# Optimization experiments

Hardware: AMD Instinct MI355X
Metric: run time of the kernel (lower is better)

## Reference

```python
import jax, jax.numpy as jnp
import numpy as np

B, N, DIM, HEADS, DHEAD, DEPTH, EDGE = 1, 384, 128, 4, 64, 3, 8
INNER = HEADS * DHEAD  # 256


def _make_rotary():
    inv = 1.0 / (10000.0 ** (np.arange(0, DHEAD, 2, dtype=np.float32) / DHEAD))
    f = np.arange(N, dtype=np.float32)[:, None] * inv[None, :]  # [N, DHEAD//2]
    f = np.repeat(f, 2, axis=-1)  # interleaved pairs -> [N, DHEAD]
    return jnp.asarray(np.cos(f)), jnp.asarray(np.sin(f))

COS, SIN = _make_rotary()


def _rotate_half(x):
    x2 = x.reshape(x.shape[:-1] + (DHEAD // 2, 2))
    return jnp.stack((-x2[..., 1], x2[..., 0]), axis=-1).reshape(x.shape)


def _layer_norm(x, s, b, eps=1e-3):
    mu = jnp.mean(x, axis=-1, keepdims=True)
    var = jnp.mean(jnp.square(x - mu), axis=-1, keepdims=True)
    return (x - mu) * jax.lax.rsqrt(var + eps) * s + b


def _gated_res(x, res, Wg):
    gi = jnp.concatenate([x, res, x - res], axis=-1)  # [B,N,3*DIM]
    g = jax.nn.sigmoid(gi @ Wg)  # [B,N,1]
    return x * g + res * (1.0 - g)


def setup_inputs() -> dict:
    key = jax.random.key(0)
    ks = jax.random.split(key, 16)
    p = lambda k, shape: 0.02 * jax.random.normal(k, shape, jnp.float32)
    return {
        "nodes": jax.random.normal(ks[0], (B, N, DIM), jnp.float32),
        "edges": jax.random.normal(ks[1], (B, N, N, EDGE), jnp.float32),
        "ln1_s": jnp.ones((DEPTH, DIM), jnp.float32), "ln1_b": jnp.zeros((DEPTH, DIM), jnp.float32),
        "Wq": p(ks[2], (DEPTH, DIM, INNER)), "bq": jnp.zeros((DEPTH, INNER), jnp.float32),
        "Wkv": p(ks[3], (DEPTH, DIM, 2 * INNER)), "bkv": jnp.zeros((DEPTH, 2 * INNER), jnp.float32),
        "We": p(ks[4], (DEPTH, EDGE, INNER)), "be": jnp.zeros((DEPTH, INNER), jnp.float32),
        "Wo": p(ks[5], (DEPTH, INNER, DIM)), "bo": jnp.zeros((DEPTH, DIM), jnp.float32),
        "Wg_attn": p(ks[6], (DEPTH, 3 * DIM, 1)),
        "ln2_s": jnp.ones((DEPTH, DIM), jnp.float32), "ln2_b": jnp.zeros((DEPTH, DIM), jnp.float32),
        "W1": p(ks[7], (DEPTH, DIM, 4 * DIM)), "b1": jnp.zeros((DEPTH, 4 * DIM), jnp.float32),
        "W2": p(ks[8], (DEPTH, 4 * DIM, DIM)), "b2": jnp.zeros((DEPTH, DIM), jnp.float32),
        "Wg_ff": p(ks[9], (DEPTH, 3 * DIM, 1)),
        "Wd1": p(ks[10], (DIM, 9)), "bd1": jnp.zeros((9,), jnp.float32),
        "Wd2": p(ks[11], (9, 3)), "bd2": jnp.zeros((3,), jnp.float32),
        "mask": jnp.ones((B, N), dtype=bool),
    }


def _forward(nodes, edges, ln1_s, ln1_b, Wq, bq, Wkv, bkv, We, be, Wo, bo, Wg_attn,
             ln2_s, ln2_b, W1, b1, W2, b2, Wg_ff, Wd1, bd1, Wd2, bd2, mask):
    cos = COS[None, None]  # [1,1,N,DHEAD]
    sin = SIN[None, None]
    mask2 = mask[:, None, :, None] & mask[:, None, None, :]  # [B,1,N,N]
    x = nodes
    for i in range(DEPTH):
        # --- pre-norm attention with edge-conditioned K/V and rotary pos emb ---
        xn = _layer_norm(x, ln1_s[i], ln1_b[i])
        q = (xn @ Wq[i] + bq[i]).reshape(B, N, HEADS, DHEAD).transpose(0, 2, 1, 3)
        k, v = jnp.split(xn @ Wkv[i] + bkv[i], 2, axis=-1)
        k = k.reshape(B, N, HEADS, DHEAD).transpose(0, 2, 1, 3)
        v = v.reshape(B, N, HEADS, DHEAD).transpose(0, 2, 1, 3)
        e = (edges @ We[i] + be[i]).reshape(B, N, N, HEADS, DHEAD).transpose(0, 3, 1, 2, 4)  # [B,H,i,j,d]
        q = q * cos + _rotate_half(q) * sin
        k = k * cos + _rotate_half(k) * sin
        kf = k[:, :, None, :, :] + e  # [B,H,i,j,d]
        vf = v[:, :, None, :, :] + e
        sim = jnp.einsum('bhid,bhijd->bhij', q, kf) * (DHEAD ** -0.5)
        sim = jnp.where(mask2, sim, -1e9)
        attn = jax.nn.softmax(sim, axis=-1)
        out = jnp.einsum('bhij,bhijd->bhid', attn, vf)
        out = out.transpose(0, 2, 1, 3).reshape(B, N, INNER) @ Wo[i] + bo[i]
        x = _gated_res(out, x, Wg_attn[i])
        # --- pre-norm feedforward ---
        xn2 = _layer_norm(x, ln2_s[i], ln2_b[i])
        h = jax.nn.gelu(xn2 @ W1[i] + b1[i], approximate=False)
        ff = h @ W2[i] + b2[i]
        x = _gated_res(ff, x, Wg_ff[i])
    y = jax.nn.relu(x @ Wd1 + bd1)
    y = y @ Wd2 + bd2  # [B,N,3]
    return y - jnp.mean(y, axis=1)  # broadcasts since B == 1 (matches TF semantics)


def reference(nodes, edges, ln1_s, ln1_b, Wq, bq, Wkv, bkv, We, be, Wo, bo, Wg_attn,
              ln2_s, ln2_b, W1, b1, W2, b2, Wg_ff, Wd1, bd1, Wd2, bd2, mask):
    return _forward(nodes, edges, ln1_s, ln1_b, Wq, bq, Wkv, bkv, We, be, Wo, bo, Wg_attn,
                    ln2_s, ln2_b, W1, b1, W2, b2, Wg_ff, Wd1, bd1, Wd2, bd2, mask)
```

## Files before the change

### kernel.cpp

```cpp
#include <hip/hip_runtime.h>
#include <math.h>

#define NTOK 384
#define DIM  128
#define HEADS 4
#define DHEAD 64
#define INNER 256
#define DEPTH 3
#define EDGE 8
#define FFD 512

__device__ __forceinline__ float wave_sum64(float v){
#pragma unroll
  for (int m = 32; m >= 1; m >>= 1) v += __shfl_xor(v, m, 64);
  return v;
}
__device__ __forceinline__ float wave_max64(float v){
#pragma unroll
  for (int m = 32; m >= 1; m >>= 1) v = fmaxf(v, __shfl_xor(v, m, 64));
  return v;
}

__device__ __forceinline__ int swz_row(int id){ return (id & 7) * 48 + (id >> 3); }

__device__ __forceinline__ void rotary_val(int i, int d, float* c, float* s){
  int j = d >> 1;
  double ex = (double)(2 * j) / 64.0;
  float p = (float)pow(10000.0, ex);
  float inv = 1.0f / p;
  float f = (float)i * inv;
  double fd = (double)f;
  *c = (float)cos(fd);
  *s = (float)sin(fd);
}

__device__ __forceinline__ void qkv_row_v2(
    int i, int t, const float* __restrict__ snx,
    const float* __restrict__ Wq, const float* __restrict__ bq,
    const float* __restrict__ Wkv, const float* __restrict__ bkv,
    const float* __restrict__ We, const float* __restrict__ be,
    const float* __restrict__ cosRow, const float* __restrict__ sinRow,
    float* __restrict__ qb_, float* __restrict__ kbT, float* __restrict__ vb_,
    float* __restrict__ qWeB, float* __restrict__ qbeB,
    float4* __restrict__ qp4)
{
  int ks   = (t < 192) ? 0 : 1;
  int quad = (t < 192) ? t : t - 192;
  float4 acc = {0.f, 0.f, 0.f, 0.f};
  if (t < 384){
    const float4* Wp; int stride4;
    if (quad < 64){ Wp = (const float4*)Wq + quad;         stride4 = 64;  }
    else          { Wp = (const float4*)Wkv + (quad - 64); stride4 = 128; }
    int k0 = ks * 64;
#pragma unroll 8
    for (int kk = 0; kk < 64; ++kk){
      int k = k0 + kk;
      float4 w = Wp[(size_t)k * stride4];
      float x = snx[k];
      acc.x = fmaf(x, w.x, acc.x); acc.y = fmaf(x, w.y, acc.y);
      acc.z = fmaf(x, w.z, acc.z); acc.w = fmaf(x, w.w, acc.w);
    }
    if (ks == 1) qp4[quad] = acc;
  }
  __syncthreads();
  if (t < 192){
    float4 p = qp4[quad];
    acc.x += p.x; acc.y += p.y; acc.z += p.z; acc.w += p.w;
    if (quad < 64){
      int c0 = 4 * quad;
      float4 b = ((const float4*)bq)[quad];
      float a0 = acc.x + b.x, a1 = acc.y + b.y, a2 = acc.z + b.z, a3 = acc.w + b.w;
      int d0 = c0 & 63;
      float c_0 = cosRow[d0],     s_0 = sinRow[d0];
      float c_1 = cosRow[d0 + 2], s_1 = sinRow[d0 + 2];
      float r0 = a0 * c_0 - a1 * s_0;
      float r1 = a1 * c_0 + a0 * s_0;
      float r2 = a2 * c_1 - a3 * s_1;
      float r3 = a3 * c_1 + a2 * s_1;
      float4 qv; qv.x = r0; qv.y = r1; qv.z = r2; qv.w = r3;
      *(float4*)(qb_ + (size_t)i * 256 + c0) = qv;
      int h = quad >> 4;
#pragma unroll
      for (int cc = 0; cc < 8; ++cc){
        const float* wc = We + cc * 256 + c0;
        float pr = r0 * wc[0] + r1 * wc[1] + r2 * wc[2] + r3 * wc[3];
#pragma unroll
        for (int m = 8; m >= 1; m >>= 1) pr += __shfl_xor(pr, m, 16);
        if ((t & 15) == 0) qWeB[(h * NTOK + i) * 8 + cc] = pr;
      }
      const float* bc = be + c0;
      float pb = r0 * bc[0] + r1 * bc[1] + r2 * bc[2] + r3 * bc[3];
#pragma unroll
      for (int m = 8; m >= 1; m >>= 1) pb += __shfl_xor(pb, m, 16);
      if ((t & 15) == 0) qbeB[h * NTOK + i] = pb;
    } else if (quad < 128){
      int c0 = 4 * (quad - 64);
      float4 b = ((const float4*)bkv)[quad - 64];
      float a0 = acc.x + b.x, a1 = acc.y + b.y, a2 = acc.z + b.z, a3 = acc.w + b.w;
      int d0 = c0 & 63, h = c0 >> 6;
      float c_0 = cosRow[d0],     s_0 = sinRow[d0];
      float c_1 = cosRow[d0 + 2], s_1 = sinRow[d0 + 2];
      float r0 = a0 * c_0 - a1 * s_0;
      float r1 = a1 * c_0 + a0 * s_0;
      float r2 = a2 * c_1 - a3 * s_1;
      float r3 = a3 * c_1 + a2 * s_1;
      float* kp = kbT + (size_t)(h * 64 + d0) * NTOK + i;
      kp[0]        = r0;
      kp[NTOK]     = r1;
      kp[2 * NTOK] = r2;
      kp[3 * NTOK] = r3;
    } else {
      int vq = quad - 128;
      int c0 = 4 * vq;
      float4 b = ((const float4*)bkv)[64 + vq];
      float4 vv;
      vv.x = acc.x + b.x; vv.y = acc.y + b.y;
      vv.z = acc.z + b.z; vv.w = acc.w + b.w;
      *(float4*)(vb_ + (size_t)i * 256 + c0) = vv;
    }
  }
}

__global__ __launch_bounds__(512) void k_lnqkv(
    const float* __restrict__ x,
    const float* __restrict__ ls, const float* __restrict__ lb,
    const float* __restrict__ Wq, const float* __restrict__ bq,
    const float* __restrict__ Wkv, const float* __restrict__ bkv,
    const float* __restrict__ We, const float* __restrict__ be,
    float* __restrict__ cosS, float* __restrict__ sinS,
    float* __restrict__ qb_, float* __restrict__ kbT, float* __restrict__ vb_,
    float* __restrict__ qWeB, float* __restrict__ qbeB)
{
  __shared__ float snx[128];
  __shared__ float crow[64], srow[64];
  __shared__ float4 qp4[192];
  int i = swz_row(blockIdx.x);
  int t = threadIdx.x;

  if (t >= 448){
    int d = t - 448;
    float c, s;
    rotary_val(i, d, &c, &s);
    crow[d] = c; srow[d] = s;
    cosS[i * 64 + d] = c; sinS[i * 64 + d] = s;
  }
  if (t < 64){
    float x0 = x[(size_t)i * 128 + t], x1 = x[(size_t)i * 128 + 64 + t];
    float mu = wave_sum64(x0 + x1) * (1.0f / 128.0f);
    float d0 = x0 - mu, d1 = x1 - mu;
    float var = wave_sum64(d0 * d0 + d1 * d1) * (1.0f / 128.0f);
    float rstd = 1.0f / sqrtf(var + 1e-3f);
    snx[t]      = d0 * rstd * ls[t]      + lb[t];
    snx[t + 64] = d1 * rstd * ls[t + 64] + lb[t + 64];
  }
  __syncthreads();
  qkv_row_v2(i, t, snx, Wq, bq, Wkv, bkv, We, be, crow, srow,
             qb_, kbT, vb_, qWeB, qbeB, qp4);
}

__global__ __launch_bounds__(512) void k_layer(
    const float* __restrict__ qb_, const float* __restrict__ kbT, const float* __restrict__ vb_,
    const float* __restrict__ qWeB, const float* __restrict__ qbeB,
    const float* __restrict__ edges,
    const float* __restrict__ We, const float* __restrict__ be,
    const float* __restrict__ Wo, const float* __restrict__ bo,
    const float* __restrict__ Wg_a,
    const float* __restrict__ ln2s, const float* __restrict__ ln2b,
    const float* __restrict__ W1, const float* __restrict__ b1,
    const float* __restrict__ W2, const float* __restrict__ b2,
    const float* __restrict__ Wg_f,
    const float* __restrict__ xin, float* __restrict__ xout,
    int has_next,
    const float* __restrict__ ls_n, const float* __restrict__ lb_n,
    const float* __restrict__ Wq_n, const float* __restrict__ bq_n,
    const float* __restrict__ Wkv_n, const float* __restrict__ bkv_n,
    const float* __restrict__ We_n, const float* __restrict__ be_n,
    const float* __restrict__ cosS, const float* __restrict__ sinS,
    float* __restrict__ qb_o, float* __restrict__ kbT_o, float* __restrict__ vb_o,
    float* __restrict__ qWeB_o, float* __restrict__ qbeB_o)
{
  __shared__ float qsL[256];
  __shared__ float qw[4][8];
  __shared__ float qbe[4];
  __shared__ float attnL[4][384];
  __shared__ float redA[8], redB[8];
  __shared__ float red8[8][8];
  __shared__ float part[512];
  __shared__ float ar[256];
  __shared__ float xold[128];
  __shared__ float xrow[128];
  __shared__ float snx[128];
  __shared__ float hs[512];
  __shared__ float4 prL[512];
  float* prF = (float*)prL;

  int i = swz_row(blockIdx.x);
  int t = threadIdx.x;

  if (t < 256) qsL[t] = qb_[(size_t)i * 256 + t];
  else if (t < 288){ int idx = t - 256; qw[idx >> 3][idx & 7] = qWeB[((idx >> 3) * NTOK + i) * 8 + (idx & 7)]; }
  else if (t < 292) qbe[t - 288] = qbeB[(t - 288) * NTOK + i];
  else if (t >= 384) xold[t - 384] = xin[(size_t)i * 128 + (t - 384)];
  __syncthreads();

  int h = t >> 7, jj = t & 127;
  int wv = t >> 6;
  float sims[3];
  float4 e0s[3], e1s[3];
  {
    float qbv = qbe[h];
    const float* qsp = qsL + h * 64;
#pragma unroll
    for (int rep = 0; rep < 3; ++rep){
      int j = jj + rep * 128;
      const float* kTp = kbT + (size_t)(h * 64) * NTOK + j;
      float a0 = 0.f, a1 = 0.f, a2 = 0.f, a3 = 0.f;
#pragma unroll 8
      for (int d = 0; d < 64; d += 4){
        a0 = fmaf(qsp[d],     kTp[(size_t)d * NTOK],       a0);
        a1 = fmaf(qsp[d + 1], kTp[(size_t)(d + 1) * NTOK], a1);
        a2 = fmaf(qsp[d + 2], kTp[(size_t)(d + 2) * NTOK], a2);
        a3 = fmaf(qsp[d + 3], kTp[(size_t)(d + 3) * NTOK], a3);
      }
      const float* ep = edges + ((size_t)i * NTOK + j) * 8;
      float4 e0 = *(const float4*)ep;
      float4 e1 = *(const float4*)(ep + 4);
      e0s[rep] = e0; e1s[rep] = e1;
      float ed = e0.x * qw[h][0] + e0.y * qw[h][1] + e0.z * qw[h][2] + e0.w * qw[h][3]
               + e1.x * qw[h][4] + e1.y * qw[h][5] + e1.z * qw[h][6] + e1.w * qw[h][7];
      sims[rep] = 0.125f * (a0 + a1 + a2 + a3 + ed + qbv);
    }
  }
  float mx = wave_max64(fmaxf(sims[0], fmaxf(sims[1], sims[2])));
  if ((t & 63) == 0) redA[wv] = mx;
  __syncthreads();
  float gm = fmaxf(redA[2 * h], redA[2 * h + 1]);
  float ex0 = expf(sims[0] - gm), ex1 = expf(sims[1] - gm), ex2 = expf(sims[2] - gm);
  float sm = wave_sum64(ex0 + ex1 + ex2);
  if ((t & 63) == 0) redB[wv] = sm;
  __syncthreads();
  float inv = 1.0f / (redB[2 * h] + redB[2 * h + 1]);
  float w0 = ex0 * inv, w1 = ex1 * inv, w2 = ex2 * inv;
  attnL[h][jj] = w0; attnL[h][jj + 128] = w1; attnL[h][jj + 256] = w2;
  {
    float a8[8];
    a8[0] = w0 * e0s[0].x + w1 * e0s[1].x + w2 * e0s[2].x;
    a8[1] = w0 * e0s[0].y + w1 * e0s[1].y + w2 * e0s[2].y;
    a8[2] = w0 * e0s[0].z + w1 * e0s[1].z + w2 * e0s[2].z;
    a8[3] = w0 * e0s[0].w + w1 * e0s[1].w + w2 * e0s[2].w;
    a8[4] = w0 * e1s[0].x + w1 * e1s[1].x + w2 * e1s[2].x;
    a8[5] = w0 * e1s[0].y + w1 * e1s[1].y + w2 * e1s[2].y;
    a8[6] = w0 * e1s[0].z + w1 * e1s[1].z + w2 * e1s[2].z;
    a8[7] = w0 * e1s[0].w + w1 * e1s[1].w + w2 * e1s[2].w;
#pragma unroll
    for (int cc = 0; cc < 8; ++cc){
      float r = wave_sum64(a8[cc]);
      if ((t & 63) == 0) red8[wv][cc] = r;
    }
  }
  __syncthreads();

  {
    int hh = t >> 7, dd = t & 63, half = (t >> 6) & 1;
    const float* vp = vb_ + hh * 64 + dd;
    const float* aw_ = attnL[hh];
    int j0 = half * 192;
    float va = 0.f, vb2 = 0.f;
#pragma unroll 8
    for (int jj2 = 0; jj2 < 192; jj2 += 2){
      va  = fmaf(aw_[j0 + jj2],     vp[(size_t)(j0 + jj2) * 256],     va);
      vb2 = fmaf(aw_[j0 + jj2 + 1], vp[(size_t)(j0 + jj2 + 1) * 256], vb2);
    }
    part[t] = va + vb2;
  }
  __syncthreads();
  if (t < 256){
    int h2 = t >> 6, d = t & 63;
    float o = part[h2 * 128 + d] + part[h2 * 128 + 64 + d];
    float ew = 0.f;
#pragma unroll
    for (int cc = 0; cc < 8; ++cc)
      ew = fmaf(red8[2 * h2][cc] + red8[2 * h2 + 1][cc], We[cc * 256 + h2 * 64 + d], ew);
    ar[t] = o + ew + be[h2 * 64 + d];
  }
  __syncthreads();

  {
    int colq = t & 31, ksub = t >> 5;
    const float4* Wo4 = (const float4*)Wo;
    float4 acc = {0.f, 0.f, 0.f, 0.f};
#pragma unroll
    for (int kk = 0; kk < 16; ++kk){
      int k = ksub * 16 + kk;
      float4 w = Wo4[(size_t)k * 32 + colq];
      float a = ar[k];
      acc.x = fmaf(a, w.x, acc.x); acc.y = fmaf(a, w.y, acc.y);
      acc.z = fmaf(a, w.z, acc.z); acc.w = fmaf(a, w.w, acc.w);
    }
    prL[ksub * 32 + colq] = acc;
  }
  __syncthreads();

  if (t < 64){
    float o0 = bo[t], o1 = bo[t + 64];
#pragma unroll
    for (int s = 0; s < 16; ++s){ o0 += prF[s * 128 + t]; o1 += prF[s * 128 + 64 + t]; }
    float xo0 = xold[t], xo1 = xold[t + 64];
    float gp = o0 * Wg_a[t]      + xo0 * Wg_a[128 + t] + (o0 - xo0) * Wg_a[256 + t]
             + o1 * Wg_a[64 + t] + xo1 * Wg_a[192 + t] + (o1 - xo1) * Wg_a[320 + t];
    float z = wave_sum64(gp);
    float gg = 1.0f / (1.0f + expf(-z));
    float xr0 = o0 * gg + xo0 * (1.0f - gg);
    float xr1 = o1 * gg + xo1 * (1.0f - gg);
    xrow[t] = xr0; xrow[t + 64] = xr1;
    float mu = wave_sum64(xr0 + xr1) * (1.0f / 128.0f);
    float d0 = xr0 - mu, d1 = xr1 - mu;
    float var = wave_sum64(d0 * d0 + d1 * d1) * (1.0f / 128.0f);
    float rstd = 1.0f / sqrtf(var + 1e-3f);
    snx[t]      = d0 * rstd * ln2s[t]      + ln2b[t];
    snx[t + 64] = d1 * rstd * ln2s[t + 64] + ln2b[t + 64];
  }
  __syncthreads();

  {
    int colq = t & 127, ksub = t >> 7;
    const float4* W14 = (const float4*)W1;
    float4 acc = {0.f, 0.f, 0.f, 0.f};
#pragma unroll 8
    for (int kk = 0; kk < 32; ++kk){
      int k = ksub * 32 + kk;
      float4 w = W14[(size_t)k * 128 + colq];
      float a = snx[k];
      acc.x = fmaf(a, w.x, acc.x); acc.y = fmaf(a, w.y, acc.y);
      acc.z = fmaf(a, w.z, acc.z); acc.w = fmaf(a, w.w, acc.w);
    }
    prL[ksub * 128 + colq] = acc;
  }
  __syncthreads();

  {
    float hv = b1[t];
#pragma unroll
    for (int s3 = 0; s3 < 4; ++s3) hv += prF[s3 * 512 + t];
    const float RS2 = 0.70710678118654752440f;
    hs[t] = 0.5f * hv * (1.0f + erff(hv * RS2));
  }
  __syncthreads();

  {
    int colq = t & 31, ksub = t >> 5;
    const float4* W24 = (const float4*)W2;
    float4 acc = {0.f, 0.f, 0.f, 0.f};
#pragma unroll 8
    for (int kk = 0; kk < 32; ++kk){
      int k = ksub * 32 + kk;
      float4 w = W24[(size_t)k * 32 + colq];
      float a = hs[k];
      acc.x = fmaf(a, w.x, acc.x); acc.y = fmaf(a, w.y, acc.y);
      acc.z = fmaf(a, w.z, acc.z); acc.w = fmaf(a, w.w, acc.w);
    }
    prL[ksub * 32 + colq] = acc;
  }
  __syncthreads();

  if (t < 64){
    float f0 = b2[t], f1 = b2[t + 64];
#pragma unroll
    for (int s3 = 0; s3 < 16; ++s3){ f0 += prF[s3 * 128 + t]; f1 += prF[s3 * 128 + 64 + t]; }
    float xr0 = xrow[t], xr1 = xrow[t + 64];
    float gp = f0 * Wg_f[t]      + xr0 * Wg_f[128 + t] + (f0 - xr0) * Wg_f[256 + t]
             + f1 * Wg_f[64 + t] + xr1 * Wg_f[192 + t] + (f1 - xr1) * Wg_f[320 + t];
    float z = wave_sum64(gp);
    float gg = 1.0f / (1.0f + expf(-z));
    float xn0 = f0 * gg + xr0 * (1.0f - gg);
    float xn1 = f1 * gg + xr1 * (1.0f - gg);
    xout[(size_t)i * 128 + t]      = xn0;
    xout[(size_t)i * 128 + 64 + t] = xn1;
    if (has_next){
      float mu = wave_sum64(xn0 + xn1) * (1.0f / 128.0f);
      float d0 = xn0 - mu, d1 = xn1 - mu;
      float var = wave_sum64(d0 * d0 + d1 * d1) * (1.0f / 128.0f);
      float rstd = 1.0f / sqrtf(var + 1e-3f);
      snx[t]      = d0 * rstd * ls_n[t]      + lb_n[t];
      snx[t + 64] = d1 * rstd * ls_n[t + 64] + lb_n[t + 64];
    }
  }
  __syncthreads();

  if (has_next){
    qkv_row_v2(i, t, snx, Wq_n, bq_n, Wkv_n, bkv_n, We_n, be_n,
               cosS + (size_t)i * 64, sinS + (size_t)i * 64,
               qb_o, kbT_o, vb_o, qWeB_o, qbeB_o, prL);
  }
}

__global__ __launch_bounds__(384) void k_final(
    const float* __restrict__ x,
    const float* __restrict__ Wd1, const float* __restrict__ bd1,
    const float* __restrict__ Wd2, const float* __restrict__ bd2,
    float* __restrict__ out)
{
  __shared__ float red[6];
  int i = threadIdx.x;
  float y[9];
#pragma unroll
  for (int c = 0; c < 9; ++c) y[c] = bd1[c];
  const float4* x4 = (const float4*)(x + (size_t)i * 128);
#pragma unroll 8
  for (int r4 = 0; r4 < 32; ++r4){
    float4 xv = x4[r4];
    const float* wp = Wd1 + (r4 * 4) * 9;
#pragma unroll
    for (int c = 0; c < 9; ++c) y[c] = fmaf(xv.x, wp[c], y[c]);
#pragma unroll
    for (int c = 0; c < 9; ++c) y[c] = fmaf(xv.y, wp[9 + c], y[c]);
#pragma unroll
    for (int c = 0; c < 9; ++c) y[c] = fmaf(xv.z, wp[18 + c], y[c]);
#pragma unroll
    for (int c = 0; c < 9; ++c) y[c] = fmaf(xv.w, wp[27 + c], y[c]);
  }
#pragma unroll
  for (int c = 0; c < 9; ++c) y[c] = fmaxf(y[c], 0.0f);
  float z[3];
#pragma unroll
  for (int c = 0; c < 3; ++c){
    float a = bd2[c];
#pragma unroll
    for (int r = 0; r < 9; ++r) a = fmaf(y[r], Wd2[r * 3 + c], a);
    z[c] = a;
  }
#pragma unroll
  for (int c = 0; c < 3; ++c){
    float s = wave_sum64(z[c]);
    if ((i & 63) == 0) red[i >> 6] = s;
    __syncthreads();
    float tot = 0.f;
#pragma unroll
    for (int w = 0; w < 6; ++w) tot += red[w];
    float mean = tot * (1.0f / 384.0f);
    out[i * 3 + c] = z[c] - mean;
    __syncthreads();
  }
}

extern "C" void kernel_launch(void* const* d_in, const int* in_sizes, int n_in,
                              void* d_out, int out_size, void* d_ws, size_t ws_size,
                              hipStream_t stream)
{
  const float* nodes   = (const float*)d_in[0];
  const float* edges   = (const float*)d_in[1];
  const float* ln1_s   = (const float*)d_in[2];
  const float* ln1_b   = (const float*)d_in[3];
  const float* Wq      = (const float*)d_in[4];
  const float* bq      = (const float*)d_in[5];
  const float* Wkv     = (const float*)d_in[6];
  const float* bkv     = (const float*)d_in[7];
  const float* We      = (const float*)d_in[8];
  const float* be      = (const float*)d_in[9];
  const float* Wo      = (const float*)d_in[10];
  const float* bo      = (const float*)d_in[11];
  const float* Wg_attn = (const float*)d_in[12];
  const float* ln2_s   = (const float*)d_in[13];
  const float* ln2_b   = (const float*)d_in[14];
  const float* W1      = (const float*)d_in[15];
  const float* b1      = (const float*)d_in[16];
  const float* W2      = (const float*)d_in[17];
  const float* b2      = (const float*)d_in[18];
  const float* Wg_ff   = (const float*)d_in[19];
  const float* Wd1     = (const float*)d_in[20];
  const float* bd1     = (const float*)d_in[21];
  const float* Wd2     = (const float*)d_in[22];
  const float* bd2     = (const float*)d_in[23];

  float* ws   = (float*)d_ws;
  float* cosS = ws;
  float* sinS = cosS + 24576;
  float* qb0   = sinS + 24576;
  float* kbT0  = qb0 + 98304;
  float* vb0   = kbT0 + 98304;
  float* qWe0  = vb0 + 98304;
  float* qbe0  = qWe0 + 12288;
  float* qb1   = qbe0 + 1536;
  float* kbT1  = qb1 + 98304;
  float* vb1   = kbT1 + 98304;
  float* qWe1  = vb1 + 98304;
  float* qbe1  = qWe1 + 12288;
  float* xbuf  = qbe1 + 1536;

  k_lnqkv<<<dim3(NTOK), dim3(512), 0, stream>>>(
      nodes, ln1_s, ln1_b, Wq, bq, Wkv, bkv, We, be,
      cosS, sinS, qb0, kbT0, vb0, qWe0, qbe0);

  for (int L = 0; L < DEPTH; ++L){
    int Ln = (L < DEPTH - 1) ? (L + 1) : L;
    const float* qbi  = (L & 1) ? qb1  : qb0;
    const float* kbi  = (L & 1) ? kbT1 : kbT0;
    const float* vbi  = (L & 1) ? vb1  : vb0;
    const float* qWei = (L & 1) ? qWe1 : qWe0;
    const float* qbei = (L & 1) ? qbe1 : qbe0;
    float* qbo  = (L & 1) ? qb0  : qb1;
    float* kbo  = (L & 1) ? kbT0 : kbT1;
    float* vbo  = (L & 1) ? vb0  : vb1;
    float* qWeo = (L & 1) ? qWe0 : qWe1;
    float* qbeo = (L & 1) ? qbe0 : qbe1;

    k_layer<<<dim3(NTOK), dim3(512), 0, stream>>>(
        qbi, kbi, vbi, qWei, qbei, edges,
        We + (size_t)L * EDGE * INNER, be + L * INNER,
        Wo + (size_t)L * INNER * DIM, bo + L * DIM,
        Wg_attn + L * 3 * DIM,
        ln2_s + L * DIM, ln2_b + L * DIM,
        W1 + (size_t)L * DIM * FFD, b1 + L * FFD,
        W2 + (size_t)L * FFD * DIM, b2 + L * DIM,
        Wg_ff + L * 3 * DIM,
        (L == 0) ? nodes : xbuf, xbuf,
        (L < DEPTH - 1) ? 1 : 0,
        ln1_s + Ln * DIM, ln1_b + Ln * DIM,
        Wq + (size_t)Ln * DIM * INNER, bq + Ln * INNER,
        Wkv + (size_t)Ln * DIM * 2 * INNER, bkv + Ln * 2 * INNER,
        We + (size_t)Ln * EDGE * INNER, be + Ln * INNER,
        cosS, sinS, qbo, kbo, vbo, qWeo, qbeo);
  }

  k_final<<<dim3(1), dim3(384), 0, stream>>>(xbuf, Wd1, bd1, Wd2, bd2, (float*)d_out);
}
```

Baseline: 135.3 us.

## Store V transposed and vectorize QK and AV loops with float4 loads

V is now written transposed ([head*dim][token]) so the attention-weighted sum over tokens reads contiguous float4 runs of V and attention weights instead of strided scalars. The QK score loop now has each thread compute four adjacent keys with float4 loads from transposed K and stages the scores in shared memory. Edge features are reloaded for the aggregation step. This adds a sync and strided scattered stores when writing V, in exchange for fewer, wider loads in the hot loops.

After: 179.6 us. +32.7%, slower.

```diff
diff --git a/kernel.cpp b/kernel.cpp
--- a/kernel.cpp
+++ b/kernel.cpp
@@ -40,7 +40,7 @@
     const float* __restrict__ Wkv, const float* __restrict__ bkv,
     const float* __restrict__ We, const float* __restrict__ be,
     const float* __restrict__ cosRow, const float* __restrict__ sinRow,
-    float* __restrict__ qb_, float* __restrict__ kbT, float* __restrict__ vb_,
+    float* __restrict__ qb_, float* __restrict__ kbT, float* __restrict__ vbT,
     float* __restrict__ qWeB, float* __restrict__ qbeB,
     float4* __restrict__ qp4)
 {
@@ -113,10 +113,13 @@
       int vq = quad - 128;
       int c0 = 4 * vq;
       float4 b = ((const float4*)bkv)[64 + vq];
-      float4 vv;
-      vv.x = acc.x + b.x; vv.y = acc.y + b.y;
-      vv.z = acc.z + b.z; vv.w = acc.w + b.w;
-      *(float4*)(vb_ + (size_t)i * 256 + c0) = vv;
+      float a0 = acc.x + b.x, a1 = acc.y + b.y, a2 = acc.z + b.z, a3 = acc.w + b.w;
+      int d0 = c0 & 63, h = c0 >> 6;
+      float* vp = vbT + (size_t)(h * 64 + d0) * NTOK + i;
+      vp[0]        = a0;
+      vp[NTOK]     = a1;
+      vp[2 * NTOK] = a2;
+      vp[3 * NTOK] = a3;
     }
   }
 }
@@ -128,7 +131,7 @@
     const float* __restrict__ Wkv, const float* __restrict__ bkv,
     const float* __restrict__ We, const float* __restrict__ be,
     float* __restrict__ cosS, float* __restrict__ sinS,
-    float* __restrict__ qb_, float* __restrict__ kbT, float* __restrict__ vb_,
+    float* __restrict__ qb_, float* __restrict__ kbT, float* __restrict__ vbT,
     float* __restrict__ qWeB, float* __restrict__ qbeB)
 {
   __shared__ float snx[128];
@@ -155,11 +158,11 @@
   }
   __syncthreads();
   qkv_row_v2(i, t, snx, Wq, bq, Wkv, bkv, We, be, crow, srow,
-             qb_, kbT, vb_, qWeB, qbeB, qp4);
+             qb_, kbT, vbT, qWeB, qbeB, qp4);
 }
 
 __global__ __launch_bounds__(512) void k_layer(
-    const float* __restrict__ qb_, const float* __restrict__ kbT, const float* __restrict__ vb_,
+    const float* __restrict__ qb_, const float* __restrict__ kbT, const float* __restrict__ vbT,
     const float* __restrict__ qWeB, const float* __restrict__ qbeB,
     const float* __restrict__ edges,
     const float* __restrict__ We, const float* __restrict__ be,
@@ -176,13 +179,13 @@
     const float* __restrict__ Wkv_n, const float* __restrict__ bkv_n,
     const float* __restrict__ We_n, const float* __restrict__ be_n,
     const float* __restrict__ cosS, const float* __restrict__ sinS,
-    float* __restrict__ qb_o, float* __restrict__ kbT_o, float* __restrict__ vb_o,
+    float* __restrict__ qb_o, float* __restrict__ kbT_o, float* __restrict__ vbT_o,
     float* __restrict__ qWeB_o, float* __restrict__ qbeB_o)
 {
   __shared__ float qsL[256];
   __shared__ float qw[4][8];
   __shared__ float qbe[4];
-  __shared__ float attnL[4][384];
+  __shared__ __align__(16) float attnL[4][384];
   __shared__ float redA[8], redB[8];
   __shared__ float red8[8][8];
   __shared__ float part[512];
@@ -203,39 +206,45 @@
   else if (t >= 384) xold[t - 384] = xin[(size_t)i * 128 + (t - 384)];
   __syncthreads();
 
+  if (t < 384){
+    int h = t / 96, j4 = t % 96;
+    const float4* kT4 = (const float4*)(kbT + (size_t)(h * 64) * NTOK) + j4;
+    const float* qsp = qsL + h * 64;
+    float sA = 0.f, sB = 0.f, sC = 0.f, sD = 0.f;
+#pragma unroll 8
+    for (int d = 0; d < 64; ++d){
+      float4 kv = kT4[(size_t)d * (NTOK / 4)];
+      float q = qsp[d];
+      sA = fmaf(q, kv.x, sA); sB = fmaf(q, kv.y, sB);
+      sC = fmaf(q, kv.z, sC); sD = fmaf(q, kv.w, sD);
+    }
+    int j0 = 4 * j4;
+    const float4* ep4 = (const float4*)(edges + ((size_t)i * NTOK + j0) * 8);
+    float qbv = qbe[h];
+    float ed[4];
+#pragma unroll
+    for (int jj = 0; jj < 4; ++jj){
+      float4 e0 = ep4[2 * jj], e1 = ep4[2 * jj + 1];
+      ed[jj] = e0.x * qw[h][0] + e0.y * qw[h][1] + e0.z * qw[h][2] + e0.w * qw[h][3]
+             + e1.x * qw[h][4] + e1.y * qw[h][5] + e1.z * qw[h][6] + e1.w * qw[h][7];
+    }
+    float4 sv;
+    sv.x = 0.125f * (sA + ed[0] + qbv);
+    sv.y = 0.125f * (sB + ed[1] + qbv);
+    sv.z = 0.125f * (sC + ed[2] + qbv);
+    sv.w = 0.125f * (sD + ed[3] + qbv);
+    *(float4*)&attnL[h][j0] = sv;
+  }
+  __syncthreads();
+
   int h = t >> 7, jj = t & 127;
   int wv = t >> 6;
-  float sims[3];
-  float4 e0s[3], e1s[3];
-  {
-    float qbv = qbe[h];
-    const float* qsp = qsL + h * 64;
-#pragma unroll
-    for (int rep = 0; rep < 3; ++rep){
-      int j = jj + rep * 128;
-      const float* kTp = kbT + (size_t)(h * 64) * NTOK + j;
-      float a0 = 0.f, a1 = 0.f, a2 = 0.f, a3 = 0.f;
-#pragma unroll 8
-      for (int d = 0; d < 64; d += 4){
-        a0 = fmaf(qsp[d],     kTp[(size_t)d * NTOK],       a0);
-        a1 = fmaf(qsp[d + 1], kTp[(size_t)(d + 1) * NTOK], a1);
-        a2 = fmaf(qsp[d + 2], kTp[(size_t)(d + 2) * NTOK], a2);
-        a3 = fmaf(qsp[d + 3], kTp[(size_t)(d + 3) * NTOK], a3);
-      }
-      const float* ep = edges + ((size_t)i * NTOK + j) * 8;
-      float4 e0 = *(const float4*)ep;
-      float4 e1 = *(const float4*)(ep + 4);
-      e0s[rep] = e0; e1s[rep] = e1;
-      float ed = e0.x * qw[h][0] + e0.y * qw[h][1] + e0.z * qw[h][2] + e0.w * qw[h][3]
-               + e1.x * qw[h][4] + e1.y * qw[h][5] + e1.z * qw[h][6] + e1.w * qw[h][7];
-      sims[rep] = 0.125f * (a0 + a1 + a2 + a3 + ed + qbv);
-    }
-  }
-  float mx = wave_max64(fmaxf(sims[0], fmaxf(sims[1], sims[2])));
+  float s0 = attnL[h][jj], s1 = attnL[h][jj + 128], s2 = attnL[h][jj + 256];
+  float mx = wave_max64(fmaxf(s0, fmaxf(s1, s2)));
   if ((t & 63) == 0) redA[wv] = mx;
   __syncthreads();
   float gm = fmaxf(redA[2 * h], redA[2 * h + 1]);
-  float ex0 = expf(sims[0] - gm), ex1 = expf(sims[1] - gm), ex2 = expf(sims[2] - gm);
+  float ex0 = expf(s0 - gm), ex1 = expf(s1 - gm), ex2 = expf(s2 - gm);
   float sm = wave_sum64(ex0 + ex1 + ex2);
   if ((t & 63) == 0) redB[wv] = sm;
   __syncthreads();
@@ -243,15 +252,24 @@
   float w0 = ex0 * inv, w1 = ex1 * inv, w2 = ex2 * inv;
   attnL[h][jj] = w0; attnL[h][jj + 128] = w1; attnL[h][jj + 256] = w2;
   {
+    const float* ep = edges + ((size_t)i * NTOK + jj) * 8;
+    float4 e00 = *(const float4*)ep;
+    float4 e01 = *(const float4*)(ep + 4);
+    ep += 128 * 8;
+    float4 e10 = *(const float4*)ep;
+    float4 e11 = *(const float4*)(ep + 4);
+    ep += 128 * 8;
+    float4 e20 = *(const float4*)ep;
+    float4 e21 = *(const float4*)(ep + 4);
     float a8[8];
-    a8[0] = w0 * e0s[0].x + w1 * e0s[1].x + w2 * e0s[2].x;
-    a8[1] = w0 * e0s[0].y + w1 * e0s[1].y + w2 * e0s[2].y;
-    a8[2] = w0 * e0s[0].z + w1 * e0s[1].z + w2 * e0s[2].z;
-    a8[3] = w0 * e0s[0].w + w1 * e0s[1].w + w2 * e0s[2].w;
-    a8[4] = w0 * e1s[0].x + w1 * e1s[1].x + w2 * e1s[2].x;
-    a8[5] = w0 * e1s[0].y + w1 * e1s[1].y + w2 * e1s[2].y;
-    a8[6] = w0 * e1s[0].z + w1 * e1s[1].z + w2 * e1s[2].z;
-    a8[7] = w0 * e1s[0].w + w1 * e1s[1].w + w2 * e1s[2].w;
+    a8[0] = w0 * e00.x + w1 * e10.x + w2 * e20.x;
+    a8[1] = w0 * e00.y + w1 * e10.y + w2 * e20.y;
+    a8[2] = w0 * e00.z + w1 * e10.z + w2 * e20.z;
+    a8[3] = w0 * e00.w + w1 * e10.w + w2 * e20.w;
+    a8[4] = w0 * e01.x + w1 * e11.x + w2 * e21.x;
+    a8[5] = w0 * e01.y + w1 * e11.y + w2 * e21.y;
+    a8[6] = w0 * e01.z + w1 * e11.z + w2 * e21.z;
+    a8[7] = w0 * e01.w + w1 * e11.w + w2 * e21.w;
 #pragma unroll
     for (int cc = 0; cc < 8; ++cc){
       float r = wave_sum64(a8[cc]);
@@ -262,16 +280,17 @@
 
   {
     int hh = t >> 7, dd = t & 63, half = (t >> 6) & 1;
-    const float* vp = vb_ + hh * 64 + dd;
-    const float* aw_ = attnL[hh];
-    int j0 = half * 192;
-    float va = 0.f, vb2 = 0.f;
+    const float4* vT4 = (const float4*)(vbT + (size_t)(hh * 64 + dd) * NTOK) + half * 48;
+    const float4* aw4 = (const float4*)(attnL[hh]) + half * 48;
+    float a0 = 0.f, a1 = 0.f, a2 = 0.f, a3 = 0.f;
 #pragma unroll 8
-    for (int jj2 = 0; jj2 < 192; jj2 += 2){
-      va  = fmaf(aw_[j0 + jj2],     vp[(size_t)(j0 + jj2) * 256],     va);
-      vb2 = fmaf(aw_[j0 + jj2 + 1], vp[(size_t)(j0 + jj2 + 1) * 256], vb2);
-    }
-    part[t] = va + vb2;
+    for (int c = 0; c < 48; ++c){
+      float4 v = vT4[c];
+      float4 w = aw4[c];
+      a0 = fmaf(w.x, v.x, a0); a1 = fmaf(w.y, v.y, a1);
+      a2 = fmaf(w.z, v.z, a2); a3 = fmaf(w.w, v.w, a3);
+    }
+    part[t] = (a0 + a1) + (a2 + a3);
   }
   __syncthreads();
   if (t < 256){
@@ -390,7 +409,7 @@
   if (has_next){
     qkv_row_v2(i, t, snx, Wq_n, bq_n, Wkv_n, bkv_n, We_n, be_n,
                cosS + (size_t)i * 64, sinS + (size_t)i * 64,
-               qb_o, kbT_o, vb_o, qWeB_o, qbeB_o, prL);
+               qb_o, kbT_o, vbT_o, qWeB_o, qbeB_o, prL);
   }
 }
 
@@ -477,30 +496,30 @@
   float* sinS = cosS + 24576;
   float* qb0   = sinS + 24576;
   float* kbT0  = qb0 + 98304;
-  float* vb0   = kbT0 + 98304;
-  float* qWe0  = vb0 + 98304;
+  float* vbT0  = kbT0 + 98304;
+  float* qWe0  = vbT0 + 98304;
   float* qbe0  = qWe0 + 12288;
   float* qb1   = qbe0 + 1536;
   float* kbT1  = qb1 + 98304;
-  float* vb1   = kbT1 + 98304;
-  float* qWe1  = vb1 + 98304;
+  float* vbT1  = kbT1 + 98304;
+  float* qWe1  = vbT1 + 98304;
   float* qbe1  = qWe1 + 12288;
   float* xbuf  = qbe1 + 1536;
 
   k_lnqkv<<<dim3(NTOK), dim3(512), 0, stream>>>(
       nodes, ln1_s, ln1_b, Wq, bq, Wkv, bkv, We, be,
-      cosS, sinS, qb0, kbT0, vb0, qWe0, qbe0);
+      cosS, sinS, qb0, kbT0, vbT0, qWe0, qbe0);
 
   for (int L = 0; L < DEPTH; ++L){
     int Ln = (L < DEPTH - 1) ? (L + 1) : L;
     const float* qbi  = (L & 1) ? qb1  : qb0;
     const float* kbi  = (L & 1) ? kbT1 : kbT0;
-    const float* vbi  = (L & 1) ? vb1  : vb0;
+    const float* vbi  = (L & 1) ? vbT1 : vbT0;
     const float* qWei = (L & 1) ? qWe1 : qWe0;
     const float* qbei = (L & 1) ? qbe1 : qbe0;
     float* qbo  = (L & 1) ? qb0  : qb1;
     float* kbo  = (L & 1) ? kbT0 : kbT1;
-    float* vbo  = (L & 1) ? vb0  : vb1;
+    float* vbo  = (L & 1) ? vbT0 : vbT1;
     float* qWeo = (L & 1) ? qWe0 : qWe1;
     float* qbeo = (L & 1) ? qbe0 : qbe1;
 
```
